# Performance work log

Hardware: AMD Instinct MI355X
Metric: run time of the kernel (lower is better)

The kernel has to match this reference:

```python
import jax, jax.numpy as jnp
import numpy as np

B = 131072      # batch
G = 8           # number of groups
GS = 8          # features per group (n_features = G*GS = 64)
K = 8           # n_basis
O = 16          # kan_out_dim
TOT = G * O     # 128, GroupKANLayer output dim
R = 10          # n_rules
FIN = 20        # fuzzy_in_dim = max(2*n_rules, 8)
EPS_BN = 1e-5


def setup_inputs() -> dict:
    key = jax.random.key(0)
    ks = jax.random.split(key, 8)
    x = jax.random.normal(ks[0], (B, G * GS), dtype=jnp.float32)
    # per-group GaussianRBF params (one shared RBF per group, applied to each feature)
    rbf_centres = jnp.tile(jnp.linspace(-3.0, 3.0, K, dtype=jnp.float32)[None, :], (G, 1))
    rbf_log_widths = jnp.zeros((G, K), dtype=jnp.float32)
    rbf_weights = jax.random.normal(ks[1], (G, K), dtype=jnp.float32) * 0.1
    rbf_linear_w = jnp.ones((G,), dtype=jnp.float32)
    # group projections: kaiming normal fan_in (relu gain sqrt(2))
    proj_W = jax.random.normal(ks[2], (G, O, GS), dtype=jnp.float32) * np.sqrt(2.0 / GS)
    proj_b = jnp.zeros((G, O), dtype=jnp.float32)
    bn1_gamma = jnp.ones((TOT,), dtype=jnp.float32)
    bn1_beta = jnp.zeros((TOT,), dtype=jnp.float32)
    # fuzzy_proj linear (xavier uniform) TOT -> FIN
    a = np.sqrt(6.0 / (TOT + FIN))
    fp_W = jax.random.uniform(ks[3], (FIN, TOT), dtype=jnp.float32, minval=-a, maxval=a)
    fp_b = jnp.zeros((FIN,), dtype=jnp.float32)
    bn2_gamma = jnp.ones((FIN,), dtype=jnp.float32)
    bn2_beta = jnp.zeros((FIN,), dtype=jnp.float32)
    # IT2 fuzzy layer params
    fz_centres = jax.random.uniform(ks[4], (R, FIN), dtype=jnp.float32, minval=-1.0, maxval=1.0)
    fz_log_su = jnp.full((R, FIN), -0.7, dtype=jnp.float32)
    fz_log_sl = jnp.full((R, FIN), -1.2, dtype=jnp.float32)
    # sparse rule head
    head_W = jax.random.normal(ks[5], (1, R), dtype=jnp.float32) * 0.05
    head_b = jnp.zeros((1,), dtype=jnp.float32)
    return {
        'x': x, 'rbf_centres': rbf_centres, 'rbf_log_widths': rbf_log_widths,
        'rbf_weights': rbf_weights, 'rbf_linear_w': rbf_linear_w,
        'proj_W': proj_W, 'proj_b': proj_b,
        'bn1_gamma': bn1_gamma, 'bn1_beta': bn1_beta,
        'fp_W': fp_W, 'fp_b': fp_b, 'bn2_gamma': bn2_gamma, 'bn2_beta': bn2_beta,
        'fz_centres': fz_centres, 'fz_log_su': fz_log_su, 'fz_log_sl': fz_log_sl,
        'head_W': head_W, 'head_b': head_b,
    }


def _batchnorm(h, gamma, beta):
    # training-mode BatchNorm1d: normalize with batch mean / biased variance
    mu = h.mean(axis=0)
    var = h.var(axis=0)
    return (h - mu) * jax.lax.rsqrt(var + EPS_BN) * gamma + beta


def _forward(x, rbf_centres, rbf_log_widths, rbf_weights, rbf_linear_w,
             proj_W, proj_b, bn1_gamma, bn1_beta, fp_W, fp_b,
             bn2_gamma, bn2_beta, fz_centres, fz_log_su, fz_log_sl,
             head_W, head_b):
    b = x.shape[0]
    xg = x.reshape(b, G, GS)                               # groups are contiguous index slices
    sigma = jnp.exp(rbf_log_widths) + 1e-6                 # [G,K]
    # Gaussian RBF over all groups/features at once: [B,G,GS,K]
    rbf = jnp.exp(-0.5 * ((xg[..., None] - rbf_centres[:, None, :]) / sigma[:, None, :]) ** 2)
    act = rbf_linear_w[None, :, None] * xg + jnp.einsum('bgfk,gk->bgf', rbf, rbf_weights)
    proj = jnp.einsum('bgf,gof->bgo', act, proj_W) + proj_b  # grouped linear, [B,G,O]
    h = _batchnorm(proj.reshape(b, TOT), bn1_gamma, bn1_beta)
    # fuzzy_proj: Linear -> BN -> GELU (torch default GELU = exact erf form)
    z = _batchnorm(h @ fp_W.T + fp_b, bn2_gamma, bn2_beta)
    z = jax.nn.gelu(z, approximate=False)                    # [B,FIN]
    # IT2 fuzzy memberships
    su = jnp.exp(fz_log_su) + 1e-6                           # [R,FIN]
    sl = jnp.minimum(jnp.exp(fz_log_sl) + 1e-6, su * 0.9)
    diff = z[:, None, :] - fz_centres[None]                  # [B,R,FIN]
    upper = jnp.exp(-0.5 * (diff / su[None]) ** 2).mean(-1)  # [B,R]
    lower = jnp.exp(-0.5 * (diff / sl[None]) ** 2).mean(-1)
    firing = 0.5 * (upper + lower)
    return firing @ head_W.T + head_b                        # [B,1]


def reference(x, rbf_centres, rbf_log_widths, rbf_weights, rbf_linear_w,
              proj_W, proj_b, bn1_gamma, bn1_beta, fp_W, fp_b,
              bn2_gamma, bn2_beta, fz_centres, fz_log_su, fz_log_sl,
              head_W, head_b):
    return _forward(x, rbf_centres, rbf_log_widths, rbf_weights, rbf_linear_w,
                    proj_W, proj_b, bn1_gamma, bn1_beta, fp_W, fp_b,
                    bn2_gamma, bn2_beta, fz_centres, fz_log_su, fz_log_sl,
                    head_W, head_b)
```

## Files before the change

### kernel.cpp

```cpp
#include <hip/hip_runtime.h>
#include <hip/hip_fp16.h>
#include <math.h>

#define B_N 131072
#define NSTRIPE1 512
#define NSTRIPE2 512

#define WS_P1   0
#define WS_P2   (NSTRIPE1 * 352)
#define WS_MT   (WS_P2 + NSTRIPE2 * 40)
#define WS_C    (WS_MT + 1280)
#define WS_NH   (WS_C + 20)
#define WS_ACTH (WS_NH + 400)
#define WS_Z    (WS_ACTH + (size_t)B_N * 32)

struct alignas(16) H8 { __half2 a, b, c, d; };

__device__ __forceinline__ float gelu_exact(float v) {
    return 0.5f * v * (1.0f + erff(v * 0.70710678118654752440f));
}

__global__ __launch_bounds__(256) void k_moments(
    const float* __restrict__ x, const float* __restrict__ cen,
    const float* __restrict__ lw, const float* __restrict__ rw,
    const float* __restrict__ linw, __half* __restrict__ act_h,
    float* __restrict__ part1)
{
    __shared__ float sAcc[4][8][44];
    const int t = threadIdx.x;
    const int g = t & 7;
    const int rl = t >> 3;

    float c_[8], nh_[8], w_[8];
#pragma unroll
    for (int k = 0; k < 8; ++k) {
        c_[k] = cen[g * 8 + k];
        float s = expf(lw[g * 8 + k]) + 1e-6f;
        nh_[k] = -0.5f / (s * s);
        w_[k] = rw[g * 8 + k];
    }
    const float lin = linw[g];
    const float c0 = c_[0], nh0 = nh_[0];
    const float delta = c_[1] - c_[0];

    bool uni = true;
#pragma unroll
    for (int k = 0; k < 8; ++k) {
        float ck = c0 + (float)k * delta;
        uni = uni && (fabsf(c_[k] - ck) <= 1e-5f * (1.0f + fabsf(ck)));
        uni = uni && (fabsf(nh_[k] - nh0) <= 1e-6f * fabsf(nh0));
    }
    const bool fast = (bool)__all((int)uni);

    float W_[8];
    float k1 = 0.0f;
    if (fast) {
        k1 = -2.0f * delta * nh0;
#pragma unroll
        for (int k = 0; k < 8; ++k) {
            float kd = (float)k * delta;
            W_[k] = w_[k] * __expf(nh0 * kd * kd);
        }
    }

    float sumA[8], P[36];
#pragma unroll
    for (int f = 0; f < 8; ++f) sumA[f] = 0.0f;
#pragma unroll
    for (int i = 0; i < 36; ++i) P[i] = 0.0f;

    if (fast) {
#pragma unroll 1
        for (int row = blockIdx.x * 32 + rl; row < B_N; row += gridDim.x * 32) {
            const float* xr = x + (size_t)row * 64 + g * 8;
            float4 v0 = *(const float4*)(xr);
            float4 v1 = *(const float4*)(xr + 4);
            float xv[8] = {v0.x, v0.y, v0.z, v0.w, v1.x, v1.y, v1.z, v1.w};
            float act[8];
#pragma unroll
            for (int f = 0; f < 8; ++f) {
                float v = xv[f];
                float dv = v - c0;
                float E0 = __expf(nh0 * dv * dv);
                float T  = __expf(k1 * dv);
                float poly = W_[7];
#pragma unroll
                for (int k = 6; k >= 0; --k) poly = poly * T + W_[k];
                act[f] = lin * v + E0 * poly;
            }
            H8 h;
            h.a = __floats2half2_rn(act[0], act[1]);
            h.b = __floats2half2_rn(act[2], act[3]);
            h.c = __floats2half2_rn(act[4], act[5]);
            h.d = __floats2half2_rn(act[6], act[7]);
            *(H8*)(act_h + (size_t)row * 64 + g * 8) = h;
            int idx = 0;
#pragma unroll
            for (int f = 0; f < 8; ++f) {
                sumA[f] += act[f];
#pragma unroll
                for (int f2 = 0; f2 <= f; ++f2) { P[idx] += act[f] * act[f2]; ++idx; }
            }
        }
    } else {
#pragma unroll 1
        for (int row = blockIdx.x * 32 + rl; row < B_N; row += gridDim.x * 32) {
            const float* xr = x + (size_t)row * 64 + g * 8;
            float4 v0 = *(const float4*)(xr);
            float4 v1 = *(const float4*)(xr + 4);
            float xv[8] = {v0.x, v0.y, v0.z, v0.w, v1.x, v1.y, v1.z, v1.w};
            float act[8];
#pragma unroll
            for (int f = 0; f < 8; ++f) {
                float v = xv[f];
                float a = lin * v;
#pragma unroll
                for (int k = 0; k < 8; ++k) {
                    float d = v - c_[k];
                    a += w_[k] * __expf(d * d * nh_[k]);
                }
                act[f] = a;
            }
            H8 h;
            h.a = __floats2half2_rn(act[0], act[1]);
            h.b = __floats2half2_rn(act[2], act[3]);
            h.c = __floats2half2_rn(act[4], act[5]);
            h.d = __floats2half2_rn(act[6], act[7]);
            *(H8*)(act_h + (size_t)row * 64 + g * 8) = h;
            int idx = 0;
#pragma unroll
            for (int f = 0; f < 8; ++f) {
                sumA[f] += act[f];
#pragma unroll
                for (int f2 = 0; f2 <= f; ++f2) { P[idx] += act[f] * act[f2]; ++idx; }
            }
        }
    }

#pragma unroll
    for (int off = 32; off >= 8; off >>= 1) {
#pragma unroll
        for (int f = 0; f < 8; ++f) sumA[f] += __shfl_down(sumA[f], off, 64);
#pragma unroll
        for (int i = 0; i < 36; ++i) P[i] += __shfl_down(P[i], off, 64);
    }
    const int wave = t >> 6, lane = t & 63;
    if (lane < 8) {
        float* dst = &sAcc[wave][lane][0];
#pragma unroll
        for (int f = 0; f < 8; ++f) dst[f] = sumA[f];
#pragma unroll
        for (int i = 0; i < 36; ++i) dst[8 + i] = P[i];
    }
    __syncthreads();
    float* S = part1 + (size_t)blockIdx.x * 352;
    for (int i = t; i < 352; i += 256) {
        int gg = i / 44, v = i % 44;
        S[i] = sAcc[0][gg][v] + sAcc[1][gg][v] + sAcc[2][gg][v] + sAcc[3][gg][v];
    }
}

__global__ __launch_bounds__(256) void k_build(
    const float* __restrict__ part1, const float* __restrict__ fpW,
    const float* __restrict__ fpb, const float* __restrict__ g1,
    const float* __restrict__ b1, const float* __restrict__ Wp,
    const float* __restrict__ pb, const float* __restrict__ lsu,
    const float* __restrict__ lsl,
    float* __restrict__ Mt, float* __restrict__ Cc, float* __restrict__ nh)
{
    __shared__ float Am[8][8];
    __shared__ float Sg[8][36];
    __shared__ float a_[128], bb_[128];
    const int t = threadIdx.x;
    for (int i = t; i < 352; i += 256) {
        const float* p = part1 + i;
        float s0 = 0.0f, s1 = 0.0f, s2 = 0.0f, s3 = 0.0f;
#pragma unroll 4
        for (int st = 0; st < NSTRIPE1; st += 4) {
            s0 += p[(st    ) * 352];
            s1 += p[(st + 1) * 352];
            s2 += p[(st + 2) * 352];
            s3 += p[(st + 3) * 352];
        }
        float m = ((s0 + s1) + (s2 + s3)) * (1.0f / B_N);
        int g = i / 44, v = i % 44;
        if (v < 8) Am[g][v] = m; else Sg[g][v - 8] = m;
    }
    __syncthreads();
    if (t < 128) {
        const int g = t >> 4;
        float wv[8];
#pragma unroll
        for (int f = 0; f < 8; ++f) wv[f] = Wp[t * 8 + f];
        float dot = 0.0f;
#pragma unroll
        for (int f = 0; f < 8; ++f) dot += wv[f] * Am[g][f];
        const float pbv = pb[t];
        const float mu = pbv + dot;
        float e2 = pbv * pbv + 2.0f * pbv * dot;
        int idx = 0;
#pragma unroll
        for (int f = 0; f < 8; ++f)
#pragma unroll
            for (int f2 = 0; f2 <= f; ++f2) {
                float c2 = (f2 == f) ? 1.0f : 2.0f;
                e2 += c2 * wv[f] * wv[f2] * Sg[g][idx]; ++idx;
            }
        const float var = fmaxf(e2 - mu * mu, 0.0f);
        const float a = g1[t] * rsqrtf(var + 1e-5f);
        a_[t] = a;
        bb_[t] = b1[t] - mu * a;
    }
    __syncthreads();
    for (int i = t; i < 1280; i += 256) {
        int gf = i / 20, j = i % 20;
        int g = gf >> 3, f = gf & 7;
        float m = 0.0f;
        for (int o = 0; o < 16; ++o) {
            int c = g * 16 + o;
            m += fpW[j * 128 + c] * a_[c] * Wp[c * 8 + f];
        }
        Mt[i] = m;
    }
    if (t < 20) {
        float cj = fpb[t];
        for (int c = 0; c < 128; ++c)
            cj += fpW[t * 128 + c] * (a_[c] * pb[c] + bb_[c]);
        Cc[t] = cj;
    }
    for (int i = t; i < 200; i += 256) {
        float su = expf(lsu[i]) + 1e-6f;
        float sl = fminf(expf(lsl[i]) + 1e-6f, 0.9f * su);
        nh[i] = -0.5f / (su * su);
        nh[200 + i] = -0.5f / (sl * sl);
    }
}

__global__ __launch_bounds__(256) void k_z(
    const __half* __restrict__ act_h, const float* __restrict__ Mt,
    const float* __restrict__ Cc, float* __restrict__ zout,
    float* __restrict__ part2)
{
    __shared__ float sRed[4][40];
    const int t = threadIdx.x;
    const int row = blockIdx.x * 256 + t;

    float zp[20];
#pragma unroll
    for (int j = 0; j < 20; ++j) zp[j] = Cc[j];

#pragma unroll 1
    for (int g = 0; g < 8; ++g) {
        const H8 h = *(const H8*)(act_h + (size_t)row * 64 + g * 8);
        float2 f0 = __half22float2(h.a), f1 = __half22float2(h.b);
        float2 f2 = __half22float2(h.c), f3 = __half22float2(h.d);
        float a[8] = {f0.x, f0.y, f1.x, f1.y, f2.x, f2.y, f3.x, f3.y};
#pragma unroll
        for (int f = 0; f < 8; ++f) {
            const float* m = Mt + (g * 8 + f) * 20;
            float av = a[f];
#pragma unroll
            for (int j = 0; j < 20; ++j) zp[j] += av * m[j];
        }
    }

#pragma unroll
    for (int j = 0; j < 20; ++j) zout[(size_t)j * B_N + row] = zp[j];

    float s_[20], q_[20];
#pragma unroll
    for (int j = 0; j < 20; ++j) { s_[j] = zp[j]; q_[j] = zp[j] * zp[j]; }
#pragma unroll
    for (int off = 32; off >= 1; off >>= 1) {
#pragma unroll
        for (int j = 0; j < 20; ++j) {
            s_[j] += __shfl_down(s_[j], off, 64);
            q_[j] += __shfl_down(q_[j], off, 64);
        }
    }
    const int wave = t >> 6, lane = t & 63;
    if (lane == 0) {
#pragma unroll
        for (int j = 0; j < 20; ++j) { sRed[wave][j] = s_[j]; sRed[wave][20 + j] = q_[j]; }
    }
    __syncthreads();
    if (t < 40)
        part2[(size_t)blockIdx.x * 40 + t] =
            sRed[0][t] + sRed[1][t] + sRed[2][t] + sRed[3][t];
}

__global__ __launch_bounds__(256) void k_out(
    const float* __restrict__ zin, const float* __restrict__ part2,
    const float* __restrict__ g2, const float* __restrict__ b2,
    const float* __restrict__ nh, const float* __restrict__ fzc,
    const float* __restrict__ hW, const float* __restrict__ hb,
    float* __restrict__ out)
{
    __shared__ float sT6[6][40];
    __shared__ float sT[40], sSc[20], sSh[20];
    const int t = threadIdx.x;
    if (t < 240) {
        const int p = t / 40, e = t - p * 40;
        float s = 0.0f;
        for (int st = p; st < NSTRIPE2; st += 6) s += part2[(size_t)st * 40 + e];
        sT6[p][e] = s;
    }
    __syncthreads();
    if (t < 40)
        sT[t] = sT6[0][t] + sT6[1][t] + sT6[2][t] + sT6[3][t] + sT6[4][t] + sT6[5][t];
    __syncthreads();
    if (t < 20) {
        float mu = sT[t] * (1.0f / B_N);
        float var = fmaxf(sT[20 + t] * (1.0f / B_N) - mu * mu, 0.0f);
        float sc = g2[t] * rsqrtf(var + 1e-5f);
        sSc[t] = sc;
        sSh[t] = b2[t] - mu * sc;
    }
    __syncthreads();

    const int row = blockIdx.x * 256 + t;
    float z[20];
#pragma unroll
    for (int j = 0; j < 20; ++j) {
        float v = zin[(size_t)j * B_N + row];
        z[j] = gelu_exact(sSc[j] * v + sSh[j]);
    }
    float acc = hb[0];
#pragma unroll 1
    for (int r = 0; r < 10; ++r) {
        float u = 0.0f, l = 0.0f;
#pragma unroll
        for (int j = 0; j < 20; ++j) {
            float cx = fzc[r * 20 + j];
            float pu = nh[r * 20 + j];
            float pl = nh[200 + r * 20 + j];
            float d = z[j] - cx;
            float dd = d * d;
            u += __expf(dd * pu);
            l += __expf(dd * pl);
        }
        acc += hW[r] * 0.025f * (u + l);
    }
    out[row] = acc;
}

extern "C" void kernel_launch(void* const* d_in, const int* in_sizes, int n_in,
                              void* d_out, int out_size, void* d_ws, size_t ws_size,
                              hipStream_t stream) {
    const float* x    = (const float*)d_in[0];
    const float* cen  = (const float*)d_in[1];
    const float* lw   = (const float*)d_in[2];
    const float* rw   = (const float*)d_in[3];
    const float* linw = (const float*)d_in[4];
    const float* Wp   = (const float*)d_in[5];
    const float* pb   = (const float*)d_in[6];
    const float* g1   = (const float*)d_in[7];
    const float* b1   = (const float*)d_in[8];
    const float* fpW  = (const float*)d_in[9];
    const float* fpb  = (const float*)d_in[10];
    const float* g2   = (const float*)d_in[11];
    const float* b2   = (const float*)d_in[12];
    const float* fzc  = (const float*)d_in[13];
    const float* lsu  = (const float*)d_in[14];
    const float* lsl  = (const float*)d_in[15];
    const float* hW   = (const float*)d_in[16];
    const float* hb   = (const float*)d_in[17];

    float* ws    = (float*)d_ws;
    float* part1 = ws + WS_P1;
    float* part2 = ws + WS_P2;
    float* Mt    = ws + WS_MT;
    float* Cc    = ws + WS_C;
    float* nh    = ws + WS_NH;
    __half* acth = (__half*)(ws + WS_ACTH);
    float* zbuf  = ws + WS_Z;
    float* outp  = (float*)d_out;

    k_moments<<<NSTRIPE1, 256, 0, stream>>>(x, cen, lw, rw, linw, acth, part1);
    k_build<<<1, 256, 0, stream>>>(part1, fpW, fpb, g1, b1, Wp, pb, lsu, lsl,
                                   Mt, Cc, nh);
    k_z<<<NSTRIPE2, 256, 0, stream>>>(acth, Mt, Cc, zbuf, part2);
    k_out<<<512, 256, 0, stream>>>(zbuf, part2, g2, b2, nh, fzc, hW, hb, outp);
}
```

Baseline: 197.3 us.

## Parallelize partial-stat reductions with transposed buffer, extra kernel and atomics

The first-pass partial moments are now written transposed, one row per statistic across 1024 blocks, and reduced by a new multi-block kernel using vectorized loads and wave shuffles. This replaces the serial 512-stripe loop inside the single-block build kernel. The second-pass stats are accumulated with atomics into 64 slots that the build kernel zeroes, so the output kernel sums 64 entries instead of 512. Moments now run on 1024 blocks, which halves rows per block. The cost is an extra kernel launch, atomic contention, and float summation order that is no longer deterministic.

```diff
diff --git a/kernel.cpp b/kernel.cpp
--- a/kernel.cpp
+++ b/kernel.cpp
@@ -3,12 +3,11 @@
 #include <math.h>
 
 #define B_N 131072
-#define NSTRIPE1 512
-#define NSTRIPE2 512
-
-#define WS_P1   0
-#define WS_P2   (NSTRIPE1 * 352)
-#define WS_MT   (WS_P2 + NSTRIPE2 * 40)
+
+#define WS_P1T  0
+#define WS_ST1  (352 * 1024)
+#define WS_ST2  (WS_ST1 + 352)
+#define WS_MT   (WS_ST2 + 2560)
 #define WS_C    (WS_MT + 1280)
 #define WS_NH   (WS_C + 20)
 #define WS_ACTH (WS_NH + 400)
@@ -24,7 +23,7 @@
     const float* __restrict__ x, const float* __restrict__ cen,
     const float* __restrict__ lw, const float* __restrict__ rw,
     const float* __restrict__ linw, __half* __restrict__ act_h,
-    float* __restrict__ part1)
+    float* __restrict__ part1t)
 {
     __shared__ float sAcc[4][8][44];
     const int t = threadIdx.x;
@@ -153,36 +152,48 @@
         for (int i = 0; i < 36; ++i) dst[8 + i] = P[i];
     }
     __syncthreads();
-    float* S = part1 + (size_t)blockIdx.x * 352;
     for (int i = t; i < 352; i += 256) {
-        int gg = i / 44, v = i % 44;
-        S[i] = sAcc[0][gg][v] + sAcc[1][gg][v] + sAcc[2][gg][v] + sAcc[3][gg][v];
+        const int gg = i / 44, v = i % 44;
+        part1t[(size_t)i * 1024 + blockIdx.x] =
+            sAcc[0][gg][v] + sAcc[1][gg][v] + sAcc[2][gg][v] + sAcc[3][gg][v];
+    }
+}
+
+__global__ __launch_bounds__(256) void k_red(
+    const float* __restrict__ part1t, float* __restrict__ stat1)
+{
+    const int t = threadIdx.x, w = t >> 6, l = t & 63;
+    const int gw = blockIdx.x * 4 + w;
+#pragma unroll 1
+    for (int e = gw; e < 352; e += 64) {
+        const float* p = part1t + (size_t)e * 1024 + l * 16;
+        float4 a = *(const float4*)(p);
+        float4 b = *(const float4*)(p + 4);
+        float4 c = *(const float4*)(p + 8);
+        float4 d = *(const float4*)(p + 12);
+        float s = ((a.x + a.y) + (a.z + a.w)) + ((b.x + b.y) + (b.z + b.w))
+                + ((c.x + c.y) + (c.z + c.w)) + ((d.x + d.y) + (d.z + d.w));
+#pragma unroll
+        for (int off = 32; off >= 1; off >>= 1) s += __shfl_down(s, off, 64);
+        if (l == 0) stat1[e] = s;
     }
 }
 
 __global__ __launch_bounds__(256) void k_build(
-    const float* __restrict__ part1, const float* __restrict__ fpW,
+    const float* __restrict__ stat1, const float* __restrict__ fpW,
     const float* __restrict__ fpb, const float* __restrict__ g1,
     const float* __restrict__ b1, const float* __restrict__ Wp,
     const float* __restrict__ pb, const float* __restrict__ lsu,
     const float* __restrict__ lsl,
-    float* __restrict__ Mt, float* __restrict__ Cc, float* __restrict__ nh)
+    float* __restrict__ Mt, float* __restrict__ Cc, float* __restrict__ nh,
+    float* __restrict__ stat2)
 {
     __shared__ float Am[8][8];
     __shared__ float Sg[8][36];
     __shared__ float a_[128], bb_[128];
     const int t = threadIdx.x;
     for (int i = t; i < 352; i += 256) {
-        const float* p = part1 + i;
-        float s0 = 0.0f, s1 = 0.0f, s2 = 0.0f, s3 = 0.0f;
-#pragma unroll 4
-        for (int st = 0; st < NSTRIPE1; st += 4) {
-            s0 += p[(st    ) * 352];
-            s1 += p[(st + 1) * 352];
-            s2 += p[(st + 2) * 352];
-            s3 += p[(st + 3) * 352];
-        }
-        float m = ((s0 + s1) + (s2 + s3)) * (1.0f / B_N);
+        float m = stat1[i] * (1.0f / B_N);
         int g = i / 44, v = i % 44;
         if (v < 8) Am[g][v] = m; else Sg[g][v - 8] = m;
     }
@@ -234,12 +245,13 @@
         nh[i] = -0.5f / (su * su);
         nh[200 + i] = -0.5f / (sl * sl);
     }
+    for (int i = t; i < 2560; i += 256) stat2[i] = 0.0f;
 }
 
 __global__ __launch_bounds__(256) void k_z(
     const __half* __restrict__ act_h, const float* __restrict__ Mt,
     const float* __restrict__ Cc, float* __restrict__ zout,
-    float* __restrict__ part2)
+    float* __restrict__ stat2)
 {
     __shared__ float sRed[4][40];
     const int t = threadIdx.x;
@@ -284,30 +296,26 @@
         for (int j = 0; j < 20; ++j) { sRed[wave][j] = s_[j]; sRed[wave][20 + j] = q_[j]; }
     }
     __syncthreads();
-    if (t < 40)
-        part2[(size_t)blockIdx.x * 40 + t] =
-            sRed[0][t] + sRed[1][t] + sRed[2][t] + sRed[3][t];
+    if (t < 40) {
+        float v = sRed[0][t] + sRed[1][t] + sRed[2][t] + sRed[3][t];
+        atomicAdd(&stat2[(blockIdx.x & 63) * 40 + t], v);
+    }
 }
 
 __global__ __launch_bounds__(256) void k_out(
-    const float* __restrict__ zin, const float* __restrict__ part2,
+    const float* __restrict__ zin, const float* __restrict__ stat2,
     const float* __restrict__ g2, const float* __restrict__ b2,
     const float* __restrict__ nh, const float* __restrict__ fzc,
     const float* __restrict__ hW, const float* __restrict__ hb,
     float* __restrict__ out)
 {
-    __shared__ float sT6[6][40];
     __shared__ float sT[40], sSc[20], sSh[20];
     const int t = threadIdx.x;
-    if (t < 240) {
-        const int p = t / 40, e = t - p * 40;
+    if (t < 40) {
         float s = 0.0f;
-        for (int st = p; st < NSTRIPE2; st += 6) s += part2[(size_t)st * 40 + e];
-        sT6[p][e] = s;
-    }
-    __syncthreads();
-    if (t < 40)
-        sT[t] = sT6[0][t] + sT6[1][t] + sT6[2][t] + sT6[3][t] + sT6[4][t] + sT6[5][t];
+        for (int st = 0; st < 64; ++st) s += stat2[st * 40 + t];
+        sT[t] = s;
+    }
     __syncthreads();
     if (t < 20) {
         float mu = sT[t] * (1.0f / B_N);
@@ -366,19 +374,21 @@
     const float* hW   = (const float*)d_in[16];
     const float* hb   = (const float*)d_in[17];
 
-    float* ws    = (float*)d_ws;
-    float* part1 = ws + WS_P1;
-    float* part2 = ws + WS_P2;
-    float* Mt    = ws + WS_MT;
-    float* Cc    = ws + WS_C;
-    float* nh    = ws + WS_NH;
-    __half* acth = (__half*)(ws + WS_ACTH);
-    float* zbuf  = ws + WS_Z;
-    float* outp  = (float*)d_out;
-
-    k_moments<<<NSTRIPE1, 256, 0, stream>>>(x, cen, lw, rw, linw, acth, part1);
-    k_build<<<1, 256, 0, stream>>>(part1, fpW, fpb, g1, b1, Wp, pb, lsu, lsl,
-                                   Mt, Cc, nh);
-    k_z<<<NSTRIPE2, 256, 0, stream>>>(acth, Mt, Cc, zbuf, part2);
-    k_out<<<512, 256, 0, stream>>>(zbuf, part2, g2, b2, nh, fzc, hW, hb, outp);
-}
+    float* ws     = (float*)d_ws;
+    float* part1t = ws + WS_P1T;
+    float* stat1  = ws + WS_ST1;
+    float* stat2  = ws + WS_ST2;
+    float* Mt     = ws + WS_MT;
+    float* Cc     = ws + WS_C;
+    float* nh     = ws + WS_NH;
+    __half* acth  = (__half*)(ws + WS_ACTH);
+    float* zbuf   = ws + WS_Z;
+    float* outp   = (float*)d_out;
+
+    k_moments<<<1024, 256, 0, stream>>>(x, cen, lw, rw, linw, acth, part1t);
+    k_red<<<16, 256, 0, stream>>>(part1t, stat1);
+    k_build<<<1, 256, 0, stream>>>(stat1, fpW, fpb, g1, b1, Wp, pb, lsu, lsl,
+                                   Mt, Cc, nh, stat2);
+    k_z<<<512, 256, 0, stream>>>(acth, Mt, Cc, zbuf, stat2);
+    k_out<<<512, 256, 0, stream>>>(zbuf, stat2, g2, b2, nh, fzc, hW, hb, outp);
+}
```

Result: faster. 166.8 us (-15.5%).
